# Kernel tuning notes

Measured on AMD Instinct MI355X. Metric: run time of the kernel, lower is better.

## Reference

```python
import math
import jax, jax.numpy as jnp
import numpy as np

B, T, D = 2, 2048, 1024
H, DH = 16, 64
DFF = int(4 * D * 2 / 3)  # 2730, as in the torch __init__
EPS = 1e-5


def _alibi_slopes(n_heads):
    def p2(n):
        start = 2 ** (-2 ** (-(math.log2(n) - 3)))
        return [start * start ** i for i in range(n)]
    if math.log2(n_heads).is_integer():
        s = p2(n_heads)
    else:
        closest = 2 ** math.floor(math.log2(n_heads))
        s = p2(closest) + p2(2 * closest)[0::2][: n_heads - closest]
    return jnp.asarray(s, dtype=jnp.float32)


def rmsnorm(x, g):
    var = jnp.mean(x * x, axis=-1, keepdims=True)
    return g * (x * jax.lax.rsqrt(var + EPS))


def setup_inputs() -> dict:
    key = jax.random.key(0)
    ks = jax.random.split(key, 9)
    sd = 0.02
    return {
        "x":  jax.random.normal(ks[0], (B, T, D), jnp.float32),
        "g1": jnp.ones((D,), jnp.float32),
        "Wq": jax.random.normal(ks[1], (D, H * DH), jnp.float32) * sd,
        "Wk": jax.random.normal(ks[2], (D, H * DH), jnp.float32) * sd,
        "Wv": jax.random.normal(ks[3], (D, H * DH), jnp.float32) * sd,
        "Wo": jax.random.normal(ks[4], (H * DH, D), jnp.float32) * sd,
        "g2": jnp.ones((D,), jnp.float32),
        "W1": jax.random.normal(ks[5], (D, DFF), jnp.float32) * sd,
        "W2": jax.random.normal(ks[6], (D, DFF), jnp.float32) * sd,
        "W3": jax.random.normal(ks[7], (DFF, D), jnp.float32) * sd,
    }


def reference(x, g1, Wq, Wk, Wv, Wo, g2, W1, W2, W3):
    scale = DH ** -0.5
    h = rmsnorm(x, g1)
    q = (h @ Wq).reshape(B, T, H, DH)
    k = (h @ Wk).reshape(B, T, H, DH)
    v = (h @ Wv).reshape(B, T, H, DH)
    # scores (B, H, T, T)
    att = jnp.einsum("bqhd,bkhd->bhqk", q, k) * scale
    # ALiBi bias as in source: dist = clamp(j - i, min=0) -> zero on causal region
    pos = jnp.arange(T)
    dist = jnp.clip(pos[None, :] - pos[:, None], 0, None).astype(jnp.float32)
    bias = -_alibi_slopes(H)[:, None, None] * dist[None, :, :]  # (H, T, T)
    causal = pos[None, :] <= pos[:, None]  # (T, T)
    neg_inf = jnp.asarray(-jnp.inf, att.dtype)
    att = jnp.where(causal[None, None], att + bias[None], neg_inf)
    p = jax.nn.softmax(att, axis=-1)
    ctx = jnp.einsum("bhqk,bkhd->bqhd", p, v).reshape(B, T, H * DH)
    x = x + ctx @ Wo
    h2 = rmsnorm(x, g2)
    x = x + (jax.nn.silu(h2 @ W1) * (h2 @ W2)) @ W3
    return x
```

## Files before the change

### kernel.cpp

```cpp
#include <hip/hip_runtime.h>
#include <hip/hip_bf16.h>
#include <cstdint>
#include <cstddef>

typedef __bf16 bf16;
typedef __attribute__((ext_vector_type(8))) __bf16 bf16x8;
typedef __attribute__((ext_vector_type(4))) float f32x4;

#define NB 2
#define NT 2048
#define ND 1024
#define NH 16
#define NDH 64
#define NBT 4096
#define NDFF 2730
#define NDFFP 2816
#define NQKV 3072
#define NFF2 5632
#define REPS 1e-5f

#define AS1 __attribute__((address_space(1)))
#define AS3 __attribute__((address_space(3)))

__device__ __forceinline__ void g2l16(const bf16* g, bf16* l) {
    __builtin_amdgcn_global_load_lds((const AS1 uint32_t*)g, (AS3 uint32_t*)l, 16, 0, 0);
}

__global__ void transpose_cast_kernel(const float* __restrict__ in, bf16* __restrict__ out,
                                      int K, int N, int Np, int Kp) {
    __shared__ float tile[32][33];
    int k0 = blockIdx.x * 32;
    int n0 = blockIdx.y * 32;
    int tx = threadIdx.x, ty = threadIdx.y;
#pragma unroll
    for (int j = 0; j < 4; ++j) {
        int k = k0 + ty + j * 8, n = n0 + tx;
        tile[ty + j * 8][tx] = (k < K && n < N) ? in[(size_t)k * N + n] : 0.0f;
    }
    __syncthreads();
#pragma unroll
    for (int j = 0; j < 4; ++j) {
        int n = n0 + ty + j * 8, k = k0 + tx;
        out[(size_t)n * Kp + k] = (bf16)tile[tx][ty + j * 8];
    }
}

__global__ void rmsnorm_kernel(const float* __restrict__ x, const float* __restrict__ g,
                               bf16* __restrict__ out) {
    int row = blockIdx.x;
    int t = threadIdx.x;
    const float4 v = reinterpret_cast<const float4*>(x + (size_t)row * ND)[t];
    float ss = v.x * v.x + v.y * v.y + v.z * v.z + v.w * v.w;
#pragma unroll
    for (int o = 32; o > 0; o >>= 1) ss += __shfl_down(ss, o, 64);
    __shared__ float red[4];
    if ((t & 63) == 0) red[t >> 6] = ss;
    __syncthreads();
    float scale = rsqrtf((red[0] + red[1] + red[2] + red[3]) * (1.0f / ND) + REPS);
    const float4 gv = reinterpret_cast<const float4*>(g)[t];
    union { bf16 b[4]; uint2 u; } pk;
    pk.b[0] = (bf16)(v.x * scale * gv.x);
    pk.b[1] = (bf16)(v.y * scale * gv.y);
    pk.b[2] = (bf16)(v.z * scale * gv.z);
    pk.b[3] = (bf16)(v.w * scale * gv.w);
    reinterpret_cast<uint2*>(out + (size_t)row * ND)[t] = pk.u;
}

template <int MODE>
__global__ __launch_bounds__(256)
void gemm_kernel(const bf16* __restrict__ A, const bf16* __restrict__ BT,
                 void* __restrict__ Cv, const float* __restrict__ res,
                 int M, int N, int K) {
    __shared__ __align__(16) bf16 As[4096];
    __shared__ __align__(16) bf16 Bs[4096];
    int m0 = blockIdx.y * 128, n0 = blockIdx.x * 128;
    int t = threadIdx.x;
    int wave = t >> 6, lane = t & 63;
    int wr = (wave >> 1) * 64, wc = (wave & 1) * 64;
    int lm = lane & 15, quad = lane >> 4;

    f32x4 acc[4][4] = {};

    int r0 = t >> 2, c0 = (t & 3) * 8;
    const bf16* Ap = A + (size_t)(m0 + r0) * K + c0;
    const bf16* Bp = BT + (size_t)(n0 + r0) * K + c0;
    bf16* asd0 = As + t * 8;
    bf16* asd1 = As + 2048 + t * 8;
    bf16* bsd0 = Bs + t * 8;
    bf16* bsd1 = Bs + 2048 + t * 8;

    for (int k0 = 0; k0 < K; k0 += 32) {
        __syncthreads();
        g2l16(Ap + k0, asd0);
        g2l16(Ap + (size_t)64 * K + k0, asd1);
        g2l16(Bp + k0, bsd0);
        g2l16(Bp + (size_t)64 * K + k0, bsd1);
        __syncthreads();
        bf16x8 af[4], bfr[4];
#pragma unroll
        for (int i = 0; i < 4; ++i)
            af[i] = *reinterpret_cast<const bf16x8*>(As + (wr + i * 16 + lm) * 32 + quad * 8);
#pragma unroll
        for (int j = 0; j < 4; ++j)
            bfr[j] = *reinterpret_cast<const bf16x8*>(Bs + (wc + j * 16 + lm) * 32 + quad * 8);
#pragma unroll
        for (int i = 0; i < 4; ++i)
#pragma unroll
            for (int j = 0; j < 4; ++j)
                acc[i][j] = __builtin_amdgcn_mfma_f32_16x16x32_bf16(af[i], bfr[j], acc[i][j], 0, 0, 0);
    }
#pragma unroll
    for (int i = 0; i < 4; ++i)
#pragma unroll
        for (int j = 0; j < 4; ++j)
#pragma unroll
            for (int r = 0; r < 4; ++r) {
                int row = m0 + wr + i * 16 + quad * 4 + r;
                int col = n0 + wc + j * 16 + lm;
                if (MODE == 0)
                    reinterpret_cast<bf16*>(Cv)[(size_t)row * N + col] = (bf16)acc[i][j][r];
                else
                    reinterpret_cast<float*>(Cv)[(size_t)row * N + col] =
                        res[(size_t)row * N + col] + acc[i][j][r];
            }
}

__global__ void vtrans_kernel(const bf16* __restrict__ qkv, bf16* __restrict__ vt) {
    int id = blockIdx.x * 256 + threadIdx.x;
    int d = id & 63;
    int rest = id >> 6;
    int tc = rest & 255;
    int bh = rest >> 8;
    int b = bh >> 4, h = bh & 15;
    const bf16* src = qkv + ((size_t)(b * NT + tc * 8)) * NQKV + 2048 + h * 64 + d;
    union { uint4 u4; bf16 e[8]; } pk;
#pragma unroll
    for (int i = 0; i < 8; ++i) pk.e[i] = src[(size_t)i * NQKV];
    *reinterpret_cast<uint4*>(vt + ((size_t)bh * 64 + d) * NT + tc * 8) = pk.u4;
}

__global__ __launch_bounds__(256, 3)
void attn_kernel(const bf16* __restrict__ qkv, const bf16* __restrict__ vt,
                 bf16* __restrict__ ctx) {
    int bh = blockIdx.x;
    int qt = 31 - (int)blockIdx.y;
    int b = bh >> 4, h = bh & 15;
    int t = threadIdx.x, w = t >> 6, lane = t & 63;
    int lm = lane & 15, quad = lane >> 4;

    __shared__ __align__(16) bf16 Ks[2 * 4096];
    __shared__ __align__(16) bf16 VTs[4 * 2048];
    __shared__ __align__(16) bf16 Ps[4 * 16 * 136];

    const bf16* qbase = qkv + ((size_t)(b * NT + qt * 64)) * NQKV + h * 64;
    const bf16* kbase = qkv + ((size_t)b * NT) * NQKV + 1024 + h * 64;
    const bf16* vtb = vt + ((size_t)bh * 64) * NT;
    bf16* psw = Ps + w * 16 * 136;

    bf16x8 aq[2];
#pragma unroll
    for (int ks = 0; ks < 2; ++ks)
        aq[ks] = *reinterpret_cast<const bf16x8*>(
            qbase + (size_t)(w * 16 + lm) * NQKV + ks * 32 + quad * 8);

    f32x4 o[4] = {};
    float mrow[4] = {-1e30f, -1e30f, -1e30f, -1e30f};
    float lrow[4] = {0.f, 0.f, 0.f, 0.f};

    int nfull = qt >> 1;
    for (int kt = 0; kt <= nfull; ++kt) {
        int k0 = kt * 128;
        bool diag = (kt == nfull);
        __syncthreads();
#pragma unroll
        for (int rep = 0; rep < 4; ++rep) {
            int idx = (rep & 1) * 256 + t;
            int row = idx >> 2, ch = idx & 3;
            g2l16(kbase + (size_t)(k0 + row) * NQKV + (rep >> 1) * 32 + ch * 8,
                  Ks + (rep >> 1) * 4096 + idx * 8);
        }
#pragma unroll
        for (int rep = 0; rep < 4; ++rep) {
            int d = t >> 2, ch = t & 3;
            g2l16(vtb + (size_t)d * NT + k0 + rep * 32 + ch * 8,
                  VTs + rep * 2048 + t * 8);
        }
        __syncthreads();

        f32x4 s[8];
#pragma unroll
        for (int j = 0; j < 8; ++j) s[j] = f32x4{0.f, 0.f, 0.f, 0.f};
#pragma unroll
        for (int ks = 0; ks < 2; ++ks)
#pragma unroll
            for (int j = 0; j < 8; ++j) {
                bf16x8 bk = *reinterpret_cast<const bf16x8*>(
                    Ks + ks * 4096 + (j * 16 + lm) * 32 + quad * 8);
                s[j] = __builtin_amdgcn_mfma_f32_16x16x32_bf16(aq[ks], bk, s[j], 0, 0, 0);
            }
        if (diag) {
#pragma unroll
            for (int j = 0; j < 8; ++j) {
                int col = k0 + j * 16 + lm;
#pragma unroll
                for (int r = 0; r < 4; ++r) {
                    int row = qt * 64 + w * 16 + quad * 4 + r;
                    s[j][r] = (col > row) ? -1e30f : s[j][r] * 0.125f;
                }
            }
        } else {
#pragma unroll
            for (int j = 0; j < 8; ++j)
#pragma unroll
                for (int r = 0; r < 4; ++r) s[j][r] *= 0.125f;
        }
        float mx[4];
#pragma unroll
        for (int r = 0; r < 4; ++r) {
            float a = fmaxf(fmaxf(s[0][r], s[1][r]), fmaxf(s[2][r], s[3][r]));
            float c = fmaxf(fmaxf(s[4][r], s[5][r]), fmaxf(s[6][r], s[7][r]));
            mx[r] = fmaxf(a, c);
        }
#pragma unroll
        for (int d = 1; d < 16; d <<= 1)
#pragma unroll
            for (int r = 0; r < 4; ++r) mx[r] = fmaxf(mx[r], __shfl_xor(mx[r], d, 64));
        float al[4];
#pragma unroll
        for (int r = 0; r < 4; ++r) {
            float mn = fmaxf(mrow[r], mx[r]);
            al[r] = __expf(mrow[r] - mn);
            mrow[r] = mn;
        }
        float rsum[4] = {0.f, 0.f, 0.f, 0.f};
#pragma unroll
        for (int j = 0; j < 8; ++j)
#pragma unroll
            for (int r = 0; r < 4; ++r) {
                float pv = __expf(s[j][r] - mrow[r]);
                s[j][r] = pv;
                rsum[r] += pv;
            }
#pragma unroll
        for (int d = 1; d < 16; d <<= 1)
#pragma unroll
            for (int r = 0; r < 4; ++r) rsum[r] += __shfl_xor(rsum[r], d, 64);
#pragma unroll
        for (int r = 0; r < 4; ++r) lrow[r] = lrow[r] * al[r] + rsum[r];
#pragma unroll
        for (int n = 0; n < 4; ++n)
#pragma unroll
            for (int r = 0; r < 4; ++r) o[n][r] *= al[r];
#pragma unroll
        for (int j = 0; j < 8; ++j)
#pragma unroll
            for (int r = 0; r < 4; ++r)
                psw[(quad * 4 + r) * 136 + j * 16 + lm] = (bf16)s[j][r];
#pragma unroll
        for (int ks2 = 0; ks2 < 4; ++ks2) {
            bf16x8 ap = *reinterpret_cast<const bf16x8*>(psw + lm * 136 + ks2 * 32 + quad * 8);
#pragma unroll
            for (int n = 0; n < 4; ++n) {
                bf16x8 bv = *reinterpret_cast<const bf16x8*>(
                    VTs + ks2 * 2048 + (n * 16 + lm) * 32 + quad * 8);
                o[n] = __builtin_amdgcn_mfma_f32_16x16x32_bf16(ap, bv, o[n], 0, 0, 0);
            }
        }
    }
#pragma unroll
    for (int n = 0; n < 4; ++n)
#pragma unroll
        for (int r = 0; r < 4; ++r) {
            int row = qt * 64 + w * 16 + quad * 4 + r;
            ctx[((size_t)(b * NT + row)) * ND + h * 64 + n * 16 + lm] =
                (bf16)(o[n][r] / lrow[r]);
        }
}

__global__ void silumul_kernel(const bf16* __restrict__ ug, bf16* __restrict__ y) {
    int i = blockIdx.x * 256 + threadIdx.x;
    int token = i / 352;
    int cc = (i - token * 352) * 8;
    const bf16* u = ug + (size_t)token * NFF2 + cc;
    union { uint4 u4; bf16 b[8]; } ub, gb, yb;
    ub.u4 = *reinterpret_cast<const uint4*>(u);
    gb.u4 = *reinterpret_cast<const uint4*>(u + NDFFP);
#pragma unroll
    for (int j = 0; j < 8; ++j) {
        float a = (float)ub.b[j], c = (float)gb.b[j];
        float s = a / (1.0f + __expf(-a));
        yb.b[j] = (bf16)(s * c);
    }
    *reinterpret_cast<uint4*>(y + (size_t)token * NDFFP + cc) = yb.u4;
}

extern "C" void kernel_launch(void* const* d_in, const int* in_sizes, int n_in,
                              void* d_out, int out_size, void* d_ws, size_t ws_size,
                              hipStream_t stream) {
    (void)in_sizes; (void)n_in; (void)out_size; (void)ws_size;
    const float* x  = (const float*)d_in[0];
    const float* g1 = (const float*)d_in[1];
    const float* Wq = (const float*)d_in[2];
    const float* Wk = (const float*)d_in[3];
    const float* Wv = (const float*)d_in[4];
    const float* Wo = (const float*)d_in[5];
    const float* g2 = (const float*)d_in[6];
    const float* W1 = (const float*)d_in[7];
    const float* W2 = (const float*)d_in[8];
    const float* W3 = (const float*)d_in[9];
    float* out = (float*)d_out;

    char* p = (char*)d_ws;
    auto take = [&](size_t n) { char* r = p; p += (n + 255) & ~(size_t)255; return r; };
    bf16* WqkvT = (bf16*)take((size_t)NQKV * ND * 2);
    bf16* WoT   = (bf16*)take((size_t)ND * ND * 2);
    bf16* W12T  = (bf16*)take((size_t)NFF2 * ND * 2);
    bf16* W3T   = (bf16*)take((size_t)ND * NDFFP * 2);
    char* big = take((size_t)NBT * ND * 2 + (size_t)NBT * NQKV * 2 +
                     (size_t)NB * NH * NDH * NT * 2 + (size_t)NBT * ND * 2);
    bf16* hb   = (bf16*)big;
    bf16* qkv  = (bf16*)(big + (size_t)NBT * ND * 2);
    bf16* vtb  = (bf16*)(big + (size_t)NBT * ND * 2 + (size_t)NBT * NQKV * 2);
    bf16* ctxb = (bf16*)(big + (size_t)NBT * ND * 2 + (size_t)NBT * NQKV * 2 +
                         (size_t)NB * NH * NDH * NT * 2);
    bf16* ug   = (bf16*)big;
    bf16* h2b  = (bf16*)take((size_t)NBT * ND * 2);
    bf16* ybuf = (bf16*)take((size_t)NBT * NDFFP * 2);

    dim3 tb(32, 8);
    transpose_cast_kernel<<<dim3(32, 32), tb, 0, stream>>>(Wq, WqkvT, ND, ND, ND, ND);
    transpose_cast_kernel<<<dim3(32, 32), tb, 0, stream>>>(Wk, WqkvT + (size_t)ND * ND, ND, ND, ND, ND);
    transpose_cast_kernel<<<dim3(32, 32), tb, 0, stream>>>(Wv, WqkvT + (size_t)2 * ND * ND, ND, ND, ND, ND);
    transpose_cast_kernel<<<dim3(32, 32), tb, 0, stream>>>(Wo, WoT, ND, ND, ND, ND);
    transpose_cast_kernel<<<dim3(32, 88), tb, 0, stream>>>(W1, W12T, ND, NDFF, NDFFP, ND);
    transpose_cast_kernel<<<dim3(32, 88), tb, 0, stream>>>(W2, W12T + (size_t)NDFFP * ND, ND, NDFF, NDFFP, ND);
    transpose_cast_kernel<<<dim3(88, 32), tb, 0, stream>>>(W3, W3T, NDFF, ND, ND, NDFFP);

    rmsnorm_kernel<<<NBT, 256, 0, stream>>>(x, g1, hb);

    gemm_kernel<0><<<dim3(24, 32), 256, 0, stream>>>(hb, WqkvT, qkv, nullptr, NBT, NQKV, ND);

    vtrans_kernel<<<2048, 256, 0, stream>>>(qkv, vtb);

    attn_kernel<<<dim3(32, 32), 256, 0, stream>>>(qkv, vtb, ctxb);

    gemm_kernel<1><<<dim3(8, 32), 256, 0, stream>>>(ctxb, WoT, out, x, NBT, ND, ND);

    rmsnorm_kernel<<<NBT, 256, 0, stream>>>(out, g2, h2b);

    gemm_kernel<0><<<dim3(44, 32), 256, 0, stream>>>(h2b, W12T, ug, nullptr, NBT, NFF2, ND);

    silumul_kernel<<<NBT * 352 / 256, 256, 0, stream>>>(ug, ybuf);

    gemm_kernel<1><<<dim3(8, 32), 256, 0, stream>>>(ybuf, W3T, out, out, NBT, ND, NDFFP);
}
```

Measured before the change: 416.7 us.

## Fuse V transpose, SiLU-gate into GEMMs, batch weight prep, use 64-wide tiles

Merges the seven weight transpose launches into one kernel. The V transpose moves into the QKV GEMM epilogue, and the SiLU*gate step into a dual-accumulator FFN GEMM. The two N=1024 GEMMs switch to 128x64 tiles so more blocks run across the CUs. Softmax now uses exp2 with a log2-folded scale. Together these cut launches and intermediate round trips through HBM; in exchange the FFN kernel uses more registers, and the QKV epilogue writes V with a scattered pattern.

```diff
diff --git a/kernel.cpp b/kernel.cpp
--- a/kernel.cpp
+++ b/kernel.cpp
@@ -16,21 +16,41 @@
 #define NDFF 2730
 #define NDFFP 2816
 #define NQKV 3072
-#define NFF2 5632
 #define REPS 1e-5f
+#define QK_SCALE_LOG2 0.1803368801111204f
 
 #define AS1 __attribute__((address_space(1)))
 #define AS3 __attribute__((address_space(3)))
 
+#if __has_builtin(__builtin_amdgcn_exp2f)
+#define EXP2F(x) __builtin_amdgcn_exp2f(x)
+#else
+#define EXP2F(x) exp2f(x)
+#endif
+
 __device__ __forceinline__ void g2l16(const bf16* g, bf16* l) {
     __builtin_amdgcn_global_load_lds((const AS1 uint32_t*)g, (AS3 uint32_t*)l, 16, 0, 0);
 }
 
-__global__ void transpose_cast_kernel(const float* __restrict__ in, bf16* __restrict__ out,
-                                      int K, int N, int Np, int Kp) {
+struct TPargs { const float* src[7]; bf16* dst[7]; };
+
+__global__ void prep_weights_kernel(TPargs a) {
     __shared__ float tile[32][33];
-    int k0 = blockIdx.x * 32;
-    int n0 = blockIdx.y * 32;
+    int bid = blockIdx.x;
+    int idx, local, tilesX, K, N;
+    if (bid < 4096) {
+        idx = bid >> 10; local = bid & 1023; tilesX = 32; K = 1024; N = 1024;
+    } else if (bid < 9728) {
+        idx = 4 + (bid - 4096) / 2816; local = (bid - 4096) % 2816;
+        tilesX = 32; K = 1024; N = 2730;
+    } else {
+        idx = 6; local = bid - 9728; tilesX = 88; K = 2730; N = 1024;
+    }
+    int Kp = tilesX * 32;
+    int k0 = (local % tilesX) * 32;
+    int n0 = (local / tilesX) * 32;
+    const float* in = a.src[idx];
+    bf16* out = a.dst[idx];
     int tx = threadIdx.x, ty = threadIdx.y;
 #pragma unroll
     for (int j = 0; j < 4; ++j) {
@@ -66,11 +86,10 @@
     reinterpret_cast<uint2*>(out + (size_t)row * ND)[t] = pk.u;
 }
 
-template <int MODE>
 __global__ __launch_bounds__(256)
-void gemm_kernel(const bf16* __restrict__ A, const bf16* __restrict__ BT,
-                 void* __restrict__ Cv, const float* __restrict__ res,
-                 int M, int N, int K) {
+void gemm_qkv_kernel(const bf16* __restrict__ A, const bf16* __restrict__ BT,
+                     bf16* __restrict__ C, bf16* __restrict__ vt) {
+    constexpr int K = ND, N = NQKV;
     __shared__ __align__(16) bf16 As[4096];
     __shared__ __align__(16) bf16 Bs[4096];
     int m0 = blockIdx.y * 128, n0 = blockIdx.x * 128;
@@ -109,6 +128,76 @@
             for (int j = 0; j < 4; ++j)
                 acc[i][j] = __builtin_amdgcn_mfma_f32_16x16x32_bf16(af[i], bfr[j], acc[i][j], 0, 0, 0);
     }
+    bool doVT = (n0 >= 2048);
+#pragma unroll
+    for (int i = 0; i < 4; ++i)
+#pragma unroll
+        for (int j = 0; j < 4; ++j) {
+            int row0 = m0 + wr + i * 16 + quad * 4;
+            int col = n0 + wc + j * 16 + lm;
+            union { uint2 u2; bf16 e[4]; } pk;
+#pragma unroll
+            for (int r = 0; r < 4; ++r) {
+                bf16 val = (bf16)acc[i][j][r];
+                C[(size_t)(row0 + r) * N + col] = val;
+                pk.e[r] = val;
+            }
+            if (doVT) {
+                int cg = col - 2048;
+                int h = cg >> 6, d = cg & 63;
+                int b = row0 >> 11, t0 = row0 & 2047;
+                *reinterpret_cast<uint2*>(vt + ((size_t)((b * 16 + h) * 64 + d)) * NT + t0) = pk.u2;
+            }
+        }
+}
+
+__global__ __launch_bounds__(256)
+void gemm_ffn_kernel(const bf16* __restrict__ A, const bf16* __restrict__ BT,
+                     bf16* __restrict__ Y) {
+    constexpr int K = ND;
+    __shared__ __align__(16) bf16 As[4096];
+    __shared__ __align__(16) bf16 Bu[4096];
+    __shared__ __align__(16) bf16 Bg[4096];
+    int m0 = blockIdx.y * 128, n0 = blockIdx.x * 128;
+    int t = threadIdx.x;
+    int wave = t >> 6, lane = t & 63;
+    int wr = (wave >> 1) * 64, wc = (wave & 1) * 64;
+    int lm = lane & 15, quad = lane >> 4;
+
+    f32x4 accU[4][4] = {};
+    f32x4 accG[4][4] = {};
+
+    int r0 = t >> 2, c0 = (t & 3) * 8;
+    const bf16* Ap = A + (size_t)(m0 + r0) * K + c0;
+    const bf16* Bup = BT + (size_t)(n0 + r0) * K + c0;
+    const bf16* Bgp = BT + (size_t)(NDFFP + n0 + r0) * K + c0;
+
+    for (int k0 = 0; k0 < K; k0 += 32) {
+        __syncthreads();
+        g2l16(Ap + k0, As + t * 8);
+        g2l16(Ap + (size_t)64 * K + k0, As + 2048 + t * 8);
+        g2l16(Bup + k0, Bu + t * 8);
+        g2l16(Bup + (size_t)64 * K + k0, Bu + 2048 + t * 8);
+        g2l16(Bgp + k0, Bg + t * 8);
+        g2l16(Bgp + (size_t)64 * K + k0, Bg + 2048 + t * 8);
+        __syncthreads();
+        bf16x8 af[4], bu[4], bg[4];
+#pragma unroll
+        for (int i = 0; i < 4; ++i)
+            af[i] = *reinterpret_cast<const bf16x8*>(As + (wr + i * 16 + lm) * 32 + quad * 8);
+#pragma unroll
+        for (int j = 0; j < 4; ++j) {
+            bu[j] = *reinterpret_cast<const bf16x8*>(Bu + (wc + j * 16 + lm) * 32 + quad * 8);
+            bg[j] = *reinterpret_cast<const bf16x8*>(Bg + (wc + j * 16 + lm) * 32 + quad * 8);
+        }
+#pragma unroll
+        for (int i = 0; i < 4; ++i)
+#pragma unroll
+            for (int j = 0; j < 4; ++j) {
+                accU[i][j] = __builtin_amdgcn_mfma_f32_16x16x32_bf16(af[i], bu[j], accU[i][j], 0, 0, 0);
+                accG[i][j] = __builtin_amdgcn_mfma_f32_16x16x32_bf16(af[i], bg[j], accG[i][j], 0, 0, 0);
+            }
+    }
 #pragma unroll
     for (int i = 0; i < 4; ++i)
 #pragma unroll
@@ -117,26 +206,59 @@
             for (int r = 0; r < 4; ++r) {
                 int row = m0 + wr + i * 16 + quad * 4 + r;
                 int col = n0 + wc + j * 16 + lm;
-                if (MODE == 0)
-                    reinterpret_cast<bf16*>(Cv)[(size_t)row * N + col] = (bf16)acc[i][j][r];
-                else
-                    reinterpret_cast<float*>(Cv)[(size_t)row * N + col] =
-                        res[(size_t)row * N + col] + acc[i][j][r];
-            }
-}
-
-__global__ void vtrans_kernel(const bf16* __restrict__ qkv, bf16* __restrict__ vt) {
-    int id = blockIdx.x * 256 + threadIdx.x;
-    int d = id & 63;
-    int rest = id >> 6;
-    int tc = rest & 255;
-    int bh = rest >> 8;
-    int b = bh >> 4, h = bh & 15;
-    const bf16* src = qkv + ((size_t)(b * NT + tc * 8)) * NQKV + 2048 + h * 64 + d;
-    union { uint4 u4; bf16 e[8]; } pk;
-#pragma unroll
-    for (int i = 0; i < 8; ++i) pk.e[i] = src[(size_t)i * NQKV];
-    *reinterpret_cast<uint4*>(vt + ((size_t)bh * 64 + d) * NT + tc * 8) = pk.u4;
+                float u = accU[i][j][r], g = accG[i][j][r];
+                float y = u / (1.0f + __expf(-u)) * g;
+                Y[(size_t)row * NDFFP + col] = (bf16)y;
+            }
+}
+
+__global__ __launch_bounds__(256)
+void gemm_n64_kernel(const bf16* __restrict__ A, const bf16* __restrict__ BT,
+                     float* __restrict__ C, const float* __restrict__ res,
+                     int N, int K) {
+    __shared__ __align__(16) bf16 As[4096];
+    __shared__ __align__(16) bf16 Bs[2048];
+    int m0 = blockIdx.y * 128, n0 = blockIdx.x * 64;
+    int t = threadIdx.x;
+    int wave = t >> 6, lane = t & 63;
+    int wr = (wave >> 1) * 64, wc = (wave & 1) * 32;
+    int lm = lane & 15, quad = lane >> 4;
+
+    f32x4 acc[4][2] = {};
+
+    int r0 = t >> 2, c0 = (t & 3) * 8;
+    const bf16* Ap = A + (size_t)(m0 + r0) * K + c0;
+    const bf16* Bp = BT + (size_t)(n0 + r0) * K + c0;
+
+    for (int k0 = 0; k0 < K; k0 += 32) {
+        __syncthreads();
+        g2l16(Ap + k0, As + t * 8);
+        g2l16(Ap + (size_t)64 * K + k0, As + 2048 + t * 8);
+        g2l16(Bp + k0, Bs + t * 8);
+        __syncthreads();
+        bf16x8 af[4], bfr[2];
+#pragma unroll
+        for (int i = 0; i < 4; ++i)
+            af[i] = *reinterpret_cast<const bf16x8*>(As + (wr + i * 16 + lm) * 32 + quad * 8);
+#pragma unroll
+        for (int j = 0; j < 2; ++j)
+            bfr[j] = *reinterpret_cast<const bf16x8*>(Bs + (wc + j * 16 + lm) * 32 + quad * 8);
+#pragma unroll
+        for (int i = 0; i < 4; ++i)
+#pragma unroll
+            for (int j = 0; j < 2; ++j)
+                acc[i][j] = __builtin_amdgcn_mfma_f32_16x16x32_bf16(af[i], bfr[j], acc[i][j], 0, 0, 0);
+    }
+#pragma unroll
+    for (int i = 0; i < 4; ++i)
+#pragma unroll
+        for (int j = 0; j < 2; ++j)
+#pragma unroll
+            for (int r = 0; r < 4; ++r) {
+                int row = m0 + wr + i * 16 + quad * 4 + r;
+                int col = n0 + wc + j * 16 + lm;
+                C[(size_t)row * N + col] = res[(size_t)row * N + col] + acc[i][j][r];
+            }
 }
 
 __global__ __launch_bounds__(256, 3)
@@ -205,14 +327,14 @@
 #pragma unroll
                 for (int r = 0; r < 4; ++r) {
                     int row = qt * 64 + w * 16 + quad * 4 + r;
-                    s[j][r] = (col > row) ? -1e30f : s[j][r] * 0.125f;
+                    s[j][r] = (col > row) ? -1e30f : s[j][r] * QK_SCALE_LOG2;
                 }
             }
         } else {
 #pragma unroll
             for (int j = 0; j < 8; ++j)
 #pragma unroll
-                for (int r = 0; r < 4; ++r) s[j][r] *= 0.125f;
+                for (int r = 0; r < 4; ++r) s[j][r] *= QK_SCALE_LOG2;
         }
         float mx[4];
 #pragma unroll
@@ -229,7 +351,7 @@
 #pragma unroll
         for (int r = 0; r < 4; ++r) {
             float mn = fmaxf(mrow[r], mx[r]);
-            al[r] = __expf(mrow[r] - mn);
+            al[r] = EXP2F(mrow[r] - mn);
             mrow[r] = mn;
         }
         float rsum[4] = {0.f, 0.f, 0.f, 0.f};
@@ -237,7 +359,7 @@
         for (int j = 0; j < 8; ++j)
 #pragma unroll
             for (int r = 0; r < 4; ++r) {
-                float pv = __expf(s[j][r] - mrow[r]);
+                float pv = EXP2F(s[j][r] - mrow[r]);
                 s[j][r] = pv;
                 rsum[r] += pv;
             }
@@ -275,23 +397,6 @@
             ctx[((size_t)(b * NT + row)) * ND + h * 64 + n * 16 + lm] =
                 (bf16)(o[n][r] / lrow[r]);
         }
-}
-
-__global__ void silumul_kernel(const bf16* __restrict__ ug, bf16* __restrict__ y) {
-    int i = blockIdx.x * 256 + threadIdx.x;
-    int token = i / 352;
-    int cc = (i - token * 352) * 8;
-    const bf16* u = ug + (size_t)token * NFF2 + cc;
-    union { uint4 u4; bf16 b[8]; } ub, gb, yb;
-    ub.u4 = *reinterpret_cast<const uint4*>(u);
-    gb.u4 = *reinterpret_cast<const uint4*>(u + NDFFP);
-#pragma unroll
-    for (int j = 0; j < 8; ++j) {
-        float a = (float)ub.b[j], c = (float)gb.b[j];
-        float s = a / (1.0f + __expf(-a));
-        yb.b[j] = (bf16)(s * c);
-    }
-    *reinterpret_cast<uint4*>(y + (size_t)token * NDFFP + cc) = yb.u4;
 }
 
 extern "C" void kernel_launch(void* const* d_in, const int* in_sizes, int n_in,
@@ -300,57 +405,44 @@
     (void)in_sizes; (void)n_in; (void)out_size; (void)ws_size;
     const float* x  = (const float*)d_in[0];
     const float* g1 = (const float*)d_in[1];
-    const float* Wq = (const float*)d_in[2];
-    const float* Wk = (const float*)d_in[3];
-    const float* Wv = (const float*)d_in[4];
-    const float* Wo = (const float*)d_in[5];
     const float* g2 = (const float*)d_in[6];
-    const float* W1 = (const float*)d_in[7];
-    const float* W2 = (const float*)d_in[8];
-    const float* W3 = (const float*)d_in[9];
     float* out = (float*)d_out;
 
     char* p = (char*)d_ws;
     auto take = [&](size_t n) { char* r = p; p += (n + 255) & ~(size_t)255; return r; };
     bf16* WqkvT = (bf16*)take((size_t)NQKV * ND * 2);
     bf16* WoT   = (bf16*)take((size_t)ND * ND * 2);
-    bf16* W12T  = (bf16*)take((size_t)NFF2 * ND * 2);
+    bf16* W12T  = (bf16*)take((size_t)2 * NDFFP * ND * 2);
     bf16* W3T   = (bf16*)take((size_t)ND * NDFFP * 2);
-    char* big = take((size_t)NBT * ND * 2 + (size_t)NBT * NQKV * 2 +
-                     (size_t)NB * NH * NDH * NT * 2 + (size_t)NBT * ND * 2);
-    bf16* hb   = (bf16*)big;
-    bf16* qkv  = (bf16*)(big + (size_t)NBT * ND * 2);
-    bf16* vtb  = (bf16*)(big + (size_t)NBT * ND * 2 + (size_t)NBT * NQKV * 2);
-    bf16* ctxb = (bf16*)(big + (size_t)NBT * ND * 2 + (size_t)NBT * NQKV * 2 +
-                         (size_t)NB * NH * NDH * NT * 2);
-    bf16* ug   = (bf16*)big;
-    bf16* h2b  = (bf16*)take((size_t)NBT * ND * 2);
-    bf16* ybuf = (bf16*)take((size_t)NBT * NDFFP * 2);
-
-    dim3 tb(32, 8);
-    transpose_cast_kernel<<<dim3(32, 32), tb, 0, stream>>>(Wq, WqkvT, ND, ND, ND, ND);
-    transpose_cast_kernel<<<dim3(32, 32), tb, 0, stream>>>(Wk, WqkvT + (size_t)ND * ND, ND, ND, ND, ND);
-    transpose_cast_kernel<<<dim3(32, 32), tb, 0, stream>>>(Wv, WqkvT + (size_t)2 * ND * ND, ND, ND, ND, ND);
-    transpose_cast_kernel<<<dim3(32, 32), tb, 0, stream>>>(Wo, WoT, ND, ND, ND, ND);
-    transpose_cast_kernel<<<dim3(32, 88), tb, 0, stream>>>(W1, W12T, ND, NDFF, NDFFP, ND);
-    transpose_cast_kernel<<<dim3(32, 88), tb, 0, stream>>>(W2, W12T + (size_t)NDFFP * ND, ND, NDFF, NDFFP, ND);
-    transpose_cast_kernel<<<dim3(88, 32), tb, 0, stream>>>(W3, W3T, NDFF, ND, ND, NDFFP);
+    bf16* hb    = (bf16*)take((size_t)NBT * ND * 2);
+    bf16* qkv   = (bf16*)take((size_t)NBT * NQKV * 2);
+    bf16* vtb   = (bf16*)take((size_t)NB * NH * NDH * NT * 2);
+    bf16* ctxb  = (bf16*)take((size_t)NBT * ND * 2);
+    bf16* h2b   = (bf16*)take((size_t)NBT * ND * 2);
+    bf16* ybuf  = qkv;
+
+    TPargs tp;
+    tp.src[0] = (const float*)d_in[2];  tp.dst[0] = WqkvT;
+    tp.src[1] = (const float*)d_in[3];  tp.dst[1] = WqkvT + (size_t)ND * ND;
+    tp.src[2] = (const float*)d_in[4];  tp.dst[2] = WqkvT + (size_t)2 * ND * ND;
+    tp.src[3] = (const float*)d_in[5];  tp.dst[3] = WoT;
+    tp.src[4] = (const float*)d_in[7];  tp.dst[4] = W12T;
+    tp.src[5] = (const float*)d_in[8];  tp.dst[5] = W12T + (size_t)NDFFP * ND;
+    tp.src[6] = (const float*)d_in[9];  tp.dst[6] = W3T;
+
+    prep_weights_kernel<<<12544, dim3(32, 8), 0, stream>>>(tp);
 
     rmsnorm_kernel<<<NBT, 256, 0, stream>>>(x, g1, hb);
 
-    gemm_kernel<0><<<dim3(24, 32), 256, 0, stream>>>(hb, WqkvT, qkv, nullptr, NBT, NQKV, ND);
-
-    vtrans_kernel<<<2048, 256, 0, stream>>>(qkv, vtb);
+    gemm_qkv_kernel<<<dim3(24, 32), 256, 0, stream>>>(hb, WqkvT, qkv, vtb);
 
     attn_kernel<<<dim3(32, 32), 256, 0, stream>>>(qkv, vtb, ctxb);
 
-    gemm_kernel<1><<<dim3(8, 32), 256, 0, stream>>>(ctxb, WoT, out, x, NBT, ND, ND);
+    gemm_n64_kernel<<<dim3(16, 32), 256, 0, stream>>>(ctxb, WoT, out, x, ND, ND);
 
     rmsnorm_kernel<<<NBT, 256, 0, stream>>>(out, g2, h2b);
 
-    gemm_kernel<0><<<dim3(44, 32), 256, 0, stream>>>(h2b, W12T, ug, nullptr, NBT, NFF2, ND);
-
-    silumul_kernel<<<NBT * 352 / 256, 256, 0, stream>>>(ug, ybuf);
-
-    gemm_kernel<1><<<dim3(8, 32), 256, 0, stream>>>(ybuf, W3T, out, out, NBT, ND, NDFFP);
-}
+    gemm_ffn_kernel<<<dim3(22, 32), 256, 0, stream>>>(h2b, W12T, ybuf);
+
+    gemm_n64_kernel<<<dim3(16, 32), 256, 0, stream>>>(ybuf, W3T, out, out, ND, NDFFP);
+}
```

Measured after the change: 414.8 us. About the same (-0.5%).
